# Kernel tuning notes

Hardware: AMD Instinct MI355X
Metric: run time of the kernel (lower is better)

Reference implementation:

```python
import jax, jax.numpy as jnp
import numpy as np


def _dwconv(x, w, pad):
    # depthwise conv, x: [B,C,H,W], w: [C,1,kh,kw]
    return jax.lax.conv_general_dilated(
        x, w, (1, 1), [(pad, pad), (pad, pad)],
        dimension_numbers=('NCHW', 'OIHW', 'NCHW'),
        feature_group_count=x.shape[1])


def _hw_to_wh(x, h, w):
    # rearrange 'b (h w) c -> b (w h) c'
    b, t, c = x.shape
    return x.reshape(b, h, w, c).transpose(0, 2, 1, 3).reshape(b, t, c)


def _wkv(decay, first, k, v):
    # Vision-RWKV WKV: decay/first [C4]; k, v [B, T, C4]
    w_neg = -jnp.exp(decay)  # RUN_CUDA applies w = -exp(w)
    u = first

    def step(carry, kv):
        p, q, o = carry
        kt, vt = kv
        no = jnp.maximum(o, u + kt)
        A = jnp.exp(o - no)
        Bx = jnp.exp(u + kt - no)
        y = (A * p + Bx * vt) / (A * q + Bx)
        no2 = jnp.maximum(o + w_neg, kt)
        A2 = jnp.exp(o + w_neg - no2)
        B2 = jnp.exp(kt - no2)
        return (A2 * p + B2 * vt, A2 * q + B2, no2), y

    Bn, T, C4 = k.shape
    init = (jnp.zeros((Bn, C4), k.dtype), jnp.zeros((Bn, C4), k.dtype),
            jnp.full((Bn, C4), -1e38, k.dtype))
    _, ys = jax.lax.scan(step, init, (jnp.swapaxes(k, 0, 1), jnp.swapaxes(v, 0, 1)))
    return jnp.swapaxes(ys, 0, 1)  # [B, T, C4]


def setup_inputs() -> dict:
    key = jax.random.key(0)
    ks = jax.random.split(key, 16)
    B, H, W, C = 8, 64, 64, 256
    T = H * W
    C4 = 4 * C
    s = 1.0 / np.sqrt(C)
    return {
        'x': jax.random.normal(ks[0], (B, T, C), jnp.float32),
        'alpha': jax.random.normal(ks[1], (4,), jnp.float32) * 0.5,
        'dw1': jax.random.normal(ks[2], (C, 1, 1, 1), jnp.float32) * s,
        'dw3': jax.random.normal(ks[3], (C, 1, 3, 3), jnp.float32) * s,
        'dw5': jax.random.normal(ks[4], (C, 1, 5, 5), jnp.float32) * s,
        'Wk': jax.random.normal(ks[5], (C, C), jnp.float32) * s,
        'Wv': jax.random.normal(ks[6], (C, C), jnp.float32) * s,
        'Wr': jax.random.normal(ks[7], (C, C), jnp.float32) * s,
        'Wf': jax.random.normal(ks[8], (C, C), jnp.float32) * s,
        'bf': jax.random.normal(ks[9], (C,), jnp.float32) * 0.02,
        'Wb': jax.random.normal(ks[10], (C, C), jnp.float32) * s,
        'bb': jax.random.normal(ks[11], (C,), jnp.float32) * 0.02,
        'spatial_decay': jax.random.normal(ks[12], (C4,), jnp.float32),
        'spatial_first': jax.random.normal(ks[13], (C4,), jnp.float32),
        'Wo': jax.random.normal(ks[14], (C, C4), jnp.float32) * (1.0 / np.sqrt(C4)),
        'h': H,
        'w': W,
    }


def reference(x, alpha, dw1, dw3, dw5, Wk, Wv, Wr, Wf, bf, Wb, bb,
              spatial_decay, spatial_first, Wo, h, w):
    B, T, C = x.shape
    # OmniShift (training path): alpha-weighted identity + depthwise 1/3/5 convs
    xi = x.reshape(B, h, w, C).transpose(0, 3, 1, 2)  # [B,C,H,W]
    xsft = (alpha[0] * xi + alpha[1] * _dwconv(xi, dw1, 0)
            + alpha[2] * _dwconv(xi, dw3, 1) + alpha[3] * _dwconv(xi, dw5, 2))
    xf = xsft.transpose(0, 2, 3, 1).reshape(B, T, C)  # [B,T,C]
    k = xf @ Wk.T
    v = xf @ Wv.T
    sr = jax.nn.sigmoid(xf @ Wr.T)
    # 1x1 conv1d over channels == linear with bias
    k1 = k @ Wf.T + bf
    v1 = v @ Wf.T + bf
    k3 = k @ Wb.T + bb
    v3 = v @ Wb.T + bb
    k2 = _hw_to_wh(k1, h, w)
    v2 = _hw_to_wh(v1, h, w)
    k4 = _hw_to_wh(k3, h, w)
    v4 = _hw_to_wh(v3, h, w)
    ks_ = jnp.concatenate([k1, k2, k3, k4], axis=2)  # [B,T,4C]
    vs_ = jnp.concatenate([v1, v2, v3, v4], axis=2)
    srs = jnp.concatenate([sr, sr, sr, sr], axis=2)
    Tf = jnp.asarray(T, x.dtype)
    xs = _wkv(spatial_decay / Tf, spatial_first / Tf, ks_, vs_)
    return (xs * srs) @ Wo.T  # [B,T,C]
```

## Files before the change

### kernel.cpp

```cpp
#include <hip/hip_runtime.h>

typedef __attribute__((ext_vector_type(8))) short bf16x8;
typedef __attribute__((ext_vector_type(4))) float f32x4;
typedef __attribute__((ext_vector_type(4))) unsigned short u16x4;
typedef __attribute__((ext_vector_type(2))) unsigned short u16x2;
typedef __attribute__((ext_vector_type(8))) unsigned short u16x8;

#define GLD16(g, l) __builtin_amdgcn_global_load_lds( \
    (const __attribute__((address_space(1))) void*)(g), \
    (__attribute__((address_space(3))) void*)(l), 16, 0, 0)

__device__ __forceinline__ unsigned short f2bf(float f) {
  unsigned u = __float_as_uint(f);
  unsigned r = u + 0x7FFFu + ((u >> 16) & 1u);
  return (unsigned short)(r >> 16);
}
__device__ __forceinline__ float bf2f(unsigned short h) {
  return __uint_as_float(((unsigned)h) << 16);
}


__global__ void k_weff(const float* __restrict__ alpha,
                       const float* __restrict__ dw1,
                       const float* __restrict__ dw3,
                       const float* __restrict__ dw5,
                       float* __restrict__ weff) {
  int tap = blockIdx.x;
  int c = threadIdx.x;
  int dy = tap / 5, dx = tap % 5;
  float v = alpha[3] * dw5[c * 25 + tap];
  if (dy >= 1 && dy <= 3 && dx >= 1 && dx <= 3)
    v += alpha[2] * dw3[c * 9 + (dy - 1) * 3 + (dx - 1)];
  if (tap == 12) v += alpha[1] * dw1[c] + alpha[0];
  weff[tap * 256 + c] = v;
}

__global__ void k_combine(const float* __restrict__ Wk,
                          const float* __restrict__ Wv,
                          const float* __restrict__ Wr,
                          const float* __restrict__ Wf,
                          const float* __restrict__ Wb,
                          const float* __restrict__ bfv,
                          const float* __restrict__ bbv,
                          short* __restrict__ wcat,
                          float* __restrict__ bias) {
  int mat = blockIdx.x >> 8;
  int i = blockIdx.x & 255;
  int j = threadIdx.x;
  if (mat == 4) {
    wcat[(size_t)(1024 + i) * 256 + j] = (short)f2bf(Wr[i * 256 + j]);
    if (j == 0) bias[1024 + i] = 0.f;
    return;
  }
  const float* Am = (mat & 1) ? Wb : Wf;
  const float* Bm = (mat < 2) ? Wk : Wv;
  const float* arow = Am + i * 256;
  float acc = 0.f;
  for (int m = 0; m < 256; ++m) acc += arow[m] * Bm[m * 256 + j];
  int newrow = ((mat & 1) << 9) + (i << 1) + (mat >> 1);
  wcat[(size_t)newrow * 256 + j] = (short)f2bf(acc);
  if (j == 0) bias[newrow] = (mat & 1) ? bbv[i] : bfv[i];
}

__global__ void k_wo(const float* __restrict__ Wo, short* __restrict__ wob) {
  int i = blockIdx.x * 256 + threadIdx.x;
  wob[i] = (short)f2bf(Wo[i]);
}

__global__ __launch_bounds__(256, 8)
void k_shift(const float* __restrict__ x, const float* __restrict__ weff,
             unsigned short* __restrict__ xf) {
  int c = threadIdx.x;
  int w0 = blockIdx.x * 8;
  int h0 = blockIdx.y * 2;
  int b = blockIdx.z;

  float wg[5][5];
#pragma unroll
  for (int dy = 0; dy < 5; ++dy)
#pragma unroll
    for (int dx = 0; dx < 5; ++dx)
      wg[dy][dx] = weff[(dy * 5 + dx) * 256 + c];

  const float* xb = x + (size_t)b * 4096 * 256 + c;
  int rowoff[6];
  bool rv[6];
#pragma unroll
  for (int r = 0; r < 6; ++r) {
    int y = h0 + r - 2;
    rv[r] = (y >= 0 && y < 64);
    int yc = y < 0 ? 0 : (y > 63 ? 63 : y);
    rowoff[r] = yc * 64 * 256;
  }

  float win[6][8];
#pragma unroll
  for (int j = -2; j <= 1; ++j) {
    int xx = w0 + j;
    int slot = j & 7;
    bool xv = (xx >= 0);
    int xc = xx < 0 ? 0 : xx;
#pragma unroll
    for (int r = 0; r < 6; ++r) {
      float v = xb[rowoff[r] + xc * 256];
      win[r][slot] = (xv && rv[r]) ? v : 0.f;
    }
  }

  unsigned short* xo = xf + ((size_t)b * 4096 + (size_t)h0 * 64) * 256 + c;
#pragma unroll
  for (int ui = 0; ui < 8; ++ui) {
    int w = w0 + ui;
    {
      int xx = w + 2;
      int slot = (ui + 2) & 7;
      bool xv = (xx < 64);
      int xc = xx > 63 ? 63 : xx;
#pragma unroll
      for (int r = 0; r < 6; ++r) {
        float v = xb[rowoff[r] + xc * 256];
        win[r][slot] = (xv && rv[r]) ? v : 0.f;
      }
    }
#pragma unroll
    for (int j = 0; j < 2; ++j) {
      float a0 = 0.f, a1 = 0.f, a2 = 0.f, a3 = 0.f, a4 = 0.f;
#pragma unroll
      for (int dx = 0; dx < 5; ++dx) {
        int slot = (ui - 2 + dx) & 7;
        a0 = fmaf(win[j + 0][slot], wg[0][dx], a0);
        a1 = fmaf(win[j + 1][slot], wg[1][dx], a1);
        a2 = fmaf(win[j + 2][slot], wg[2][dx], a2);
        a3 = fmaf(win[j + 3][slot], wg[3][dx], a3);
        a4 = fmaf(win[j + 4][slot], wg[4][dx], a4);
      }
      xo[((size_t)j * 64 + w) * 256] = f2bf(((a0 + a1) + (a2 + a3)) + a4);
    }
  }
}

template <int EPI, int BM, int BK>
__global__ __launch_bounds__(256, (BK == 128) ? 3 : 4)
void gemm_bt(const short* __restrict__ A, const short* __restrict__ Bm,
             const float* __restrict__ bias,
             void* __restrict__ O0, void* __restrict__ O1,
             int M, int N, int K) {
  constexpr int AE = BM * BK;
  constexpr int MI = BM / 32;
  constexpr int CH = BK / 8;
  constexpr int LA = BM * BK / 2048;
  constexpr int LB = BK / 16;
  constexpr int RW = 132;
  __shared__ __align__(16) short lds[AE + 128 * BK];

  int t = threadIdx.x;
  int lane = t & 63, wv = t >> 6;
  int wr = wv >> 1, wc = wv & 1;
  int m0 = blockIdx.x * BM, n0 = blockIdx.y * 128;
  f32x4 acc[MI][4] = {};

  for (int k0 = 0; k0 < K; k0 += BK) {
#pragma unroll
    for (int i = 0; i < LA; ++i) {
      int cc = t + i * 256;
      int row = cc / CH, kc = cc % CH;
      GLD16(A + (size_t)(m0 + row) * K + k0 + ((kc ^ (row & (CH - 1))) << 3), &lds[cc * 8]);
    }
#pragma unroll
    for (int i = 0; i < LB; ++i) {
      int cc = t + i * 256;
      int row = cc / CH, kc = cc % CH;
      GLD16(Bm + (size_t)(n0 + row) * K + k0 + ((kc ^ (row & (CH - 1))) << 3), &lds[AE + cc * 8]);
    }
    __syncthreads();
#pragma unroll
    for (int kk = 0; kk < BK / 32; ++kk) {
      int ch = kk * 4 + (lane >> 4);
      bf16x8 av[MI], bv[4];
#pragma unroll
      for (int i = 0; i < MI; ++i) {
        int row = wr * (BM / 2) + i * 16 + (lane & 15);
        av[i] = *(const bf16x8*)&lds[row * BK + ((ch ^ (row & (CH - 1))) << 3)];
      }
#pragma unroll
      for (int i = 0; i < 4; ++i) {
        int row = wc * 64 + i * 16 + (lane & 15);
        bv[i] = *(const bf16x8*)&lds[AE + row * BK + ((ch ^ (row & (CH - 1))) << 3)];
      }
#pragma unroll
      for (int mi = 0; mi < MI; ++mi)
#pragma unroll
        for (int ni = 0; ni < 4; ++ni)
          acc[mi][ni] = __builtin_amdgcn_mfma_f32_16x16x32_bf16(av[mi], bv[ni], acc[mi][ni], 0, 0, 0);
    }
    __syncthreads();
  }

  float* fl = (float*)lds;
  float bb[4];
  if (EPI == 0) {
#pragma unroll
    for (int ni = 0; ni < 4; ++ni)
      bb[ni] = bias[n0 + wc * 64 + ni * 16 + (lane & 15)];
  }
  int rrow = t >> 3;
  int colb = (t & 7) * 16;
#pragma unroll
  for (int mi = 0; mi < MI; ++mi) {
    if (mi) __syncthreads();
    {
      int r0 = (lane >> 4) * 4;
#pragma unroll
      for (int ni = 0; ni < 4; ++ni) {
        int colL = wc * 64 + (lane & 15) + ni * 16;
        f32x4 v = acc[mi][ni];
#pragma unroll
        for (int j = 0; j < 4; ++j) {
          float vj = v[j];
          if (EPI == 0) vj += bb[ni];
          fl[(wr * 16 + r0 + j) * RW + colL] = vj;
        }
      }
    }
    __syncthreads();
    float vv[16];
#pragma unroll
    for (int q = 0; q < 4; ++q)
      *(f32x4*)&vv[q * 4] = *(const f32x4*)&fl[rrow * RW + colb + q * 4];
    int grow = m0 + (rrow >> 4) * (BM / 2) + mi * 16 + (rrow & 15);
    if (EPI == 0) {
      u16x8 o0, o1;
      if (n0 < 1024) {
#pragma unroll
        for (int q = 0; q < 8; ++q) { o0[q] = f2bf(vv[q]); o1[q] = f2bf(vv[8 + q]); }
        unsigned short* dst = (unsigned short*)O0 + (size_t)grow * 1024 + n0 + colb;
        *(u16x8*)dst = o0;
        *(u16x8*)(dst + 8) = o1;
      } else {
#pragma unroll
        for (int q = 0; q < 8; ++q) {
          o0[q] = f2bf(1.f / (1.f + __expf(-vv[q])));
          o1[q] = f2bf(1.f / (1.f + __expf(-vv[8 + q])));
        }
        unsigned short* dst = (unsigned short*)O1 + (size_t)grow * 256 + (n0 - 1024) + colb;
        *(u16x8*)dst = o0;
        *(u16x8*)(dst + 8) = o1;
      }
    } else {
      float* dst = (float*)O0 + (size_t)grow * N + n0 + colb;
#pragma unroll
      for (int q = 0; q < 4; ++q) {
        f32x4 ov = {vv[q * 4], vv[q * 4 + 1], vv[q * 4 + 2], vv[q * 4 + 3]};
        *(f32x4*)(dst + q * 4) = ov;
      }
    }
  }
}

__global__ __launch_bounds__(256, 8)
void k_wkv(const unsigned short* __restrict__ kvb, const unsigned short* __restrict__ srb,
           const float* __restrict__ decay, const float* __restrict__ first,
           unsigned short* __restrict__ xssr) {
  const int T = 4096;
  int tid = threadIdx.x;
  int g = tid >> 7;
  int l = tid & 127;
  int c0 = l * 2;
  int tr = blockIdx.y;
  int s = (g << 1) | tr;
  int scol = s * 256;
  int chunk = blockIdx.x;
  int b = blockIdx.z;
  const float invT = 1.0f / 4096.0f;

  float P0 = 0.f, P1 = 0.f, Q0 = 0.f, Q1 = 0.f;
  float D0 = __expf(-__expf(decay[scol + c0] * invT));
  float D1 = __expf(-__expf(decay[scol + c0 + 1] * invT));
  float eu0 = __expf(first[scol + c0] * invT);
  float eu1 = __expf(first[scol + c0 + 1] * invT);

  int t0 = chunk * 32;
  int tstart = t0 >= 16 ? t0 - 16 : 0;
  int tend = t0 + 32;
  const size_t bT = (size_t)b * T;
  const int kvoff = (g << 9) + (c0 << 1);

  auto kvload = [&](int tt) {
    int tok = tr ? (((tt & 63) << 6) | (tt >> 6)) : tt;
    return *(const u16x4*)(kvb + (bT + tok) * 1024 + kvoff);
  };
  auto srload = [&](int tt) {
    return *(const u16x2*)(srb + (bT + tt) * 256 + c0);
  };

  u16x4 kvA = kvload(tstart);
  u16x4 kvB = kvload(tstart + 1);
  u16x2 svA = srload(tstart);
  u16x2 svB = srload(tstart + 1);

  for (int tt = tstart; tt < tend; tt += 2) {
    int tp2 = tt + 2 < tend ? tt + 2 : tend - 1;
    int tp3 = tt + 3 < tend ? tt + 3 : tend - 1;
    u16x4 kvC = kvload(tp2);
    u16x4 kvD = kvload(tp3);
    u16x2 svC = srload(tp2);
    u16x2 svD = srload(tp3);

#pragma unroll
    for (int u = 0; u < 2; ++u) {
      int ti = tt + u;
      u16x4 kv4 = u ? kvB : kvA;
      u16x2 sv = u ? svB : svA;
      float k0 = bf2f(kv4[0]), v0 = bf2f(kv4[1]);
      float k1 = bf2f(kv4[2]), v1 = bf2f(kv4[3]);
      float e0 = __expf(k0), e1 = __expf(k1);
      if (ti >= t0) {
        float t0e = e0 * eu0, t1e = e1 * eu1;
        float y0 = fmaf(t0e, v0, P0) * __builtin_amdgcn_rcpf(Q0 + t0e);
        float y1 = fmaf(t1e, v1, P1) * __builtin_amdgcn_rcpf(Q1 + t1e);
        u16x2 ow;
        ow[0] = f2bf(y0 * bf2f(sv[0]));
        ow[1] = f2bf(y1 * bf2f(sv[1]));
        *(u16x2*)(xssr + (bT + ti) * 1024 + scol + c0) = ow;
      }
      P0 = fmaf(P0, D0, e0 * v0);
      Q0 = fmaf(Q0, D0, e0);
      P1 = fmaf(P1, D1, e1 * v1);
      Q1 = fmaf(Q1, D1, e1);
    }
    kvA = kvC; kvB = kvD;
    svA = svC; svB = svD;
  }
}

extern "C" void kernel_launch(void* const* d_in, const int* in_sizes, int n_in,
                              void* d_out, int out_size, void* d_ws, size_t ws_size,
                              hipStream_t stream) {
  const float* x      = (const float*)d_in[0];
  const float* alpha  = (const float*)d_in[1];
  const float* dw1    = (const float*)d_in[2];
  const float* dw3    = (const float*)d_in[3];
  const float* dw5    = (const float*)d_in[4];
  const float* Wk     = (const float*)d_in[5];
  const float* Wv     = (const float*)d_in[6];
  const float* Wr     = (const float*)d_in[7];
  const float* Wf     = (const float*)d_in[8];
  const float* bfv    = (const float*)d_in[9];
  const float* Wb     = (const float*)d_in[10];
  const float* bbv    = (const float*)d_in[11];
  const float* sdecay = (const float*)d_in[12];
  const float* sfirst = (const float*)d_in[13];
  const float* Wo     = (const float*)d_in[14];
  (void)n_in; (void)out_size; (void)ws_size;

  const int Bn = in_sizes[0] / (4096 * 256);
  const int MT = Bn * 4096;

  char* ws = (char*)d_ws;
  size_t off = 0;
  auto alloc = [&](size_t bytes) {
    void* p = ws + off;
    off += (bytes + 255) & ~(size_t)255;
    return p;
  };
  short* xf            = (short*)alloc((size_t)MT * 256 * 2);
  unsigned short* kv   = (unsigned short*)alloc((size_t)MT * 1024 * 2);
  unsigned short* srb  = (unsigned short*)alloc((size_t)MT * 256 * 2);
  unsigned short* xssr = (unsigned short*)alloc((size_t)MT * 1024 * 2);
  short* wcat          = (short*)alloc((size_t)1280 * 256 * 2);
  float* bias          = (float*)alloc(1280 * 4);
  float* weff          = (float*)alloc(25 * 256 * 4);
  short* wob           = (short*)alloc((size_t)256 * 1024 * 2);

  k_weff<<<25, 256, 0, stream>>>(alpha, dw1, dw3, dw5, weff);
  k_combine<<<1280, 256, 0, stream>>>(Wk, Wv, Wr, Wf, Wb, bfv, bbv, wcat, bias);
  k_wo<<<1024, 256, 0, stream>>>(Wo, wob);
  k_shift<<<dim3(8, 32, Bn), 256, 0, stream>>>(x, weff, (unsigned short*)xf);
  gemm_bt<0, 128, 64><<<dim3(MT / 128, 10), 256, 0, stream>>>(xf, wcat, bias, kv, srb, MT, 1280, 256);
  k_wkv<<<dim3(128, 2, Bn), 256, 0, stream>>>(kv, srb, sdecay, sfirst, xssr);
  gemm_bt<1, 64, 128><<<dim3(MT / 64, 2), 256, 0, stream>>>((const short*)xssr, wob, nullptr, d_out, nullptr, MT, 256, 1024);
}
```

Baseline: 167.3 us.

## Replace LDS-staged GEMM with direct global-to-register MFMA loads and double buffering

Both projection GEMMs stop staging A and B tiles through shared memory with global_load_lds and barriers. Each wave now loads its MFMA fragments straight from global memory into registers, using a two-stage register double buffer that overlaps the next k-slice's loads with the current MFMAs. Shared memory is kept only for the epilogue transpose. The output GEMM also changes its tile from 64 to 128 rows, which halves its block count. The risk is that operands no longer shared across waves are fetched redundantly from global/L2, with less coalesced 16-byte accesses and higher register pressure.

```diff
diff --git a/kernel.cpp b/kernel.cpp
--- a/kernel.cpp
+++ b/kernel.cpp
@@ -5,10 +5,6 @@
 typedef __attribute__((ext_vector_type(4))) unsigned short u16x4;
 typedef __attribute__((ext_vector_type(2))) unsigned short u16x2;
 typedef __attribute__((ext_vector_type(8))) unsigned short u16x8;
-
-#define GLD16(g, l) __builtin_amdgcn_global_load_lds( \
-    (const __attribute__((address_space(1))) void*)(g), \
-    (__attribute__((address_space(3))) void*)(l), 16, 0, 0)
 
 __device__ __forceinline__ unsigned short f2bf(float f) {
   unsigned u = __float_as_uint(f);
@@ -139,64 +135,55 @@
   }
 }
 
-template <int EPI, int BM, int BK>
-__global__ __launch_bounds__(256, (BK == 128) ? 3 : 4)
-void gemm_bt(const short* __restrict__ A, const short* __restrict__ Bm,
-             const float* __restrict__ bias,
-             void* __restrict__ O0, void* __restrict__ O1,
-             int M, int N, int K) {
-  constexpr int AE = BM * BK;
-  constexpr int MI = BM / 32;
-  constexpr int CH = BK / 8;
-  constexpr int LA = BM * BK / 2048;
-  constexpr int LB = BK / 16;
+template <int EPI, int KDIM>
+__global__ __launch_bounds__(256, 3)
+void gemm_direct(const short* __restrict__ A, const short* __restrict__ Bm,
+                 const float* __restrict__ bias,
+                 void* __restrict__ O0, void* __restrict__ O1, int N) {
+  constexpr int K = KDIM;
+  constexpr int NK = K / 32;
   constexpr int RW = 132;
-  __shared__ __align__(16) short lds[AE + 128 * BK];
+  __shared__ __align__(16) float fl[32 * RW];
 
   int t = threadIdx.x;
   int lane = t & 63, wv = t >> 6;
   int wr = wv >> 1, wc = wv & 1;
-  int m0 = blockIdx.x * BM, n0 = blockIdx.y * 128;
-  f32x4 acc[MI][4] = {};
-
-  for (int k0 = 0; k0 < K; k0 += BK) {
-#pragma unroll
-    for (int i = 0; i < LA; ++i) {
-      int cc = t + i * 256;
-      int row = cc / CH, kc = cc % CH;
-      GLD16(A + (size_t)(m0 + row) * K + k0 + ((kc ^ (row & (CH - 1))) << 3), &lds[cc * 8]);
-    }
-#pragma unroll
-    for (int i = 0; i < LB; ++i) {
-      int cc = t + i * 256;
-      int row = cc / CH, kc = cc % CH;
-      GLD16(Bm + (size_t)(n0 + row) * K + k0 + ((kc ^ (row & (CH - 1))) << 3), &lds[AE + cc * 8]);
-    }
-    __syncthreads();
-#pragma unroll
-    for (int kk = 0; kk < BK / 32; ++kk) {
-      int ch = kk * 4 + (lane >> 4);
-      bf16x8 av[MI], bv[4];
-#pragma unroll
-      for (int i = 0; i < MI; ++i) {
-        int row = wr * (BM / 2) + i * 16 + (lane & 15);
-        av[i] = *(const bf16x8*)&lds[row * BK + ((ch ^ (row & (CH - 1))) << 3)];
-      }
-#pragma unroll
-      for (int i = 0; i < 4; ++i) {
-        int row = wc * 64 + i * 16 + (lane & 15);
-        bv[i] = *(const bf16x8*)&lds[AE + row * BK + ((ch ^ (row & (CH - 1))) << 3)];
-      }
-#pragma unroll
-      for (int mi = 0; mi < MI; ++mi)
-#pragma unroll
-        for (int ni = 0; ni < 4; ++ni)
-          acc[mi][ni] = __builtin_amdgcn_mfma_f32_16x16x32_bf16(av[mi], bv[ni], acc[mi][ni], 0, 0, 0);
-    }
-    __syncthreads();
-  }
-
-  float* fl = (float*)lds;
+  int m0 = blockIdx.x * 128, n0 = blockIdx.y * 128;
+  f32x4 acc[4][4] = {};
+
+  const short* Ap = A + (size_t)(m0 + wr * 64 + (lane & 15)) * K + (lane >> 4) * 8;
+  const short* Bp = Bm + (size_t)(n0 + wc * 64 + (lane & 15)) * K + (lane >> 4) * 8;
+
+  bf16x8 aA[4], bA[4], aB[4], bB[4];
+
+#define LOADF(av, bv, kk)                                              \
+  _Pragma("unroll")                                                    \
+  for (int i = 0; i < 4; ++i) {                                        \
+    av[i] = *(const bf16x8*)(Ap + (size_t)i * 16 * K + (kk) * 32);     \
+    bv[i] = *(const bf16x8*)(Bp + (size_t)i * 16 * K + (kk) * 32);     \
+  }
+#define MM(av, bv)                                                     \
+  _Pragma("unroll")                                                    \
+  for (int mi = 0; mi < 4; ++mi) {                                     \
+    _Pragma("unroll")                                                  \
+    for (int ni = 0; ni < 4; ++ni)                                     \
+      acc[mi][ni] = __builtin_amdgcn_mfma_f32_16x16x32_bf16(           \
+          av[mi], bv[ni], acc[mi][ni], 0, 0, 0);                       \
+  }
+
+  LOADF(aA, bA, 0);
+  for (int kk = 0; kk < NK - 2; kk += 2) {
+    LOADF(aB, bB, kk + 1);
+    MM(aA, bA);
+    LOADF(aA, bA, kk + 2);
+    MM(aB, bB);
+  }
+  LOADF(aB, bB, NK - 1);
+  MM(aA, bA);
+  MM(aB, bB);
+#undef LOADF
+#undef MM
+
   float bb[4];
   if (EPI == 0) {
 #pragma unroll
@@ -206,7 +193,7 @@
   int rrow = t >> 3;
   int colb = (t & 7) * 16;
 #pragma unroll
-  for (int mi = 0; mi < MI; ++mi) {
+  for (int mi = 0; mi < 4; ++mi) {
     if (mi) __syncthreads();
     {
       int r0 = (lane >> 4) * 4;
@@ -227,7 +214,7 @@
 #pragma unroll
     for (int q = 0; q < 4; ++q)
       *(f32x4*)&vv[q * 4] = *(const f32x4*)&fl[rrow * RW + colb + q * 4];
-    int grow = m0 + (rrow >> 4) * (BM / 2) + mi * 16 + (rrow & 15);
+    int grow = m0 + (rrow >> 4) * 64 + mi * 16 + (rrow & 15);
     if (EPI == 0) {
       u16x8 o0, o1;
       if (n0 < 1024) {
@@ -376,7 +363,9 @@
   k_combine<<<1280, 256, 0, stream>>>(Wk, Wv, Wr, Wf, Wb, bfv, bbv, wcat, bias);
   k_wo<<<1024, 256, 0, stream>>>(Wo, wob);
   k_shift<<<dim3(8, 32, Bn), 256, 0, stream>>>(x, weff, (unsigned short*)xf);
-  gemm_bt<0, 128, 64><<<dim3(MT / 128, 10), 256, 0, stream>>>(xf, wcat, bias, kv, srb, MT, 1280, 256);
+  gemm_direct<0, 256><<<dim3(MT / 128, 10), 256, 0, stream>>>(
+      xf, wcat, bias, kv, srb, 1280);
   k_wkv<<<dim3(128, 2, Bn), 256, 0, stream>>>(kv, srb, sdecay, sfirst, xssr);
-  gemm_bt<1, 64, 128><<<dim3(MT / 64, 2), 256, 0, stream>>>((const short*)xssr, wob, nullptr, d_out, nullptr, MT, 256, 1024);
-}
+  gemm_direct<1, 1024><<<dim3(MT / 128, 2), 256, 0, stream>>>(
+      (const short*)xssr, wob, nullptr, d_out, nullptr, 256);
+}
```

Result: slower. 254.3 us (+52.0%).

## Keep full-K A tile resident in LDS and sweep all N tiles per block

Applied to the files above, without the earlier changes.

Replaces the first projection GEMM with a dedicated kernel. Each block loads its 128-row A tile (full K=256) into LDS once, then loops over the ten 128-column B tiles, prefetching the next B tile while the current epilogue runs. The epilogue goes through an LDS staging buffer so bias add, bf16 conversion and sigmoid are written as coalesced 16-byte stores. This removes the tenfold re-read of A across column blocks, at the cost of about 145KB of LDS per block, which allows only one 4-wave block per CU and gives little latency hiding during the MFMA phase.

```diff
diff --git a/kernel.cpp b/kernel.cpp
--- a/kernel.cpp
+++ b/kernel.cpp
@@ -135,6 +135,117 @@
         a4 = fmaf(win[j + 4][slot], wg[4][dx], a4);
       }
       xo[((size_t)j * 64 + w) * 256] = f2bf(((a0 + a1) + (a2 + a3)) + a4);
+    }
+  }
+}
+
+__global__ __launch_bounds__(256, 1)
+void k_gemm1(const short* __restrict__ A, const short* __restrict__ Bm,
+             const float* __restrict__ bias,
+             unsigned short* __restrict__ kv, unsigned short* __restrict__ srb) {
+  __shared__ __align__(16) short AB[65536];
+  __shared__ __align__(16) float flb[4][16 * 66];
+
+  int t = threadIdx.x;
+  int lane = t & 63, wv = t >> 6;
+  int wr = wv >> 1, wc = wv & 1;
+  int m0 = blockIdx.x * 128;
+
+#pragma unroll
+  for (int i = 0; i < 16; ++i) {
+    int cc = t + i * 256;
+    int row = cc >> 5, kc = cc & 31;
+    GLD16(A + (size_t)(m0 + row) * 256 + ((kc ^ (row & 31)) << 3), &AB[cc * 8]);
+  }
+#pragma unroll
+  for (int i = 0; i < 16; ++i) {
+    int cc = t + i * 256;
+    int row = cc >> 5, kc = cc & 31;
+    GLD16(Bm + (size_t)row * 256 + ((kc ^ (row & 31)) << 3), &AB[32768 + cc * 8]);
+  }
+  asm volatile("s_waitcnt vmcnt(0)" ::: "memory");
+  __builtin_amdgcn_s_barrier();
+
+  float* flw = flb[wv];
+
+#pragma unroll 1
+  for (int nt = 0; nt < 10; ++nt) {
+    int n0 = nt * 128;
+    if (nt) {
+      asm volatile("s_waitcnt vmcnt(8)" ::: "memory");
+      __builtin_amdgcn_s_barrier();
+    }
+    float bb[4];
+#pragma unroll
+    for (int ni = 0; ni < 4; ++ni)
+      bb[ni] = bias[n0 + wc * 64 + ni * 16 + (lane & 15)];
+
+    f32x4 acc[4][4] = {};
+#pragma unroll
+    for (int kk = 0; kk < 8; ++kk) {
+      int ch = kk * 4 + (lane >> 4);
+      bf16x8 av[4], bv[4];
+#pragma unroll
+      for (int i = 0; i < 4; ++i) {
+        int row = wr * 64 + i * 16 + (lane & 15);
+        av[i] = *(const bf16x8*)&AB[row * 256 + ((ch ^ (row & 31)) << 3)];
+      }
+#pragma unroll
+      for (int i = 0; i < 4; ++i) {
+        int row = wc * 64 + i * 16 + (lane & 15);
+        bv[i] = *(const bf16x8*)&AB[32768 + row * 256 + ((ch ^ (row & 31)) << 3)];
+      }
+#pragma unroll
+      for (int mi = 0; mi < 4; ++mi)
+#pragma unroll
+        for (int ni = 0; ni < 4; ++ni)
+          acc[mi][ni] = __builtin_amdgcn_mfma_f32_16x16x32_bf16(av[mi], bv[ni], acc[mi][ni], 0, 0, 0);
+    }
+    asm volatile("s_waitcnt lgkmcnt(0)" ::: "memory");
+    __builtin_amdgcn_s_barrier();
+
+    if (nt < 9) {
+      int n1 = n0 + 128;
+#pragma unroll
+      for (int i = 0; i < 16; ++i) {
+        int cc = t + i * 256;
+        int row = cc >> 5, kc = cc & 31;
+        GLD16(Bm + (size_t)(n1 + row) * 256 + ((kc ^ (row & 31)) << 3),
+              &AB[32768 + cc * 8]);
+      }
+    }
+
+#pragma unroll
+    for (int mi = 0; mi < 4; ++mi) {
+      int g = lane >> 4;
+#pragma unroll
+      for (int ni = 0; ni < 4; ++ni) {
+        f32x4 v = acc[mi][ni];
+#pragma unroll
+        for (int j = 0; j < 4; ++j)
+          flw[(g * 4 + j) * 66 + ni * 16 + (lane & 15)] = v[j] + bb[ni];
+      }
+      asm volatile("s_waitcnt lgkmcnt(0)" ::: "memory");
+#pragma unroll
+      for (int rp = 0; rp < 2; ++rp) {
+        int r = (lane >> 3) + rp * 8;
+        int c0 = (lane & 7) * 8;
+        float vv[8];
+#pragma unroll
+        for (int q = 0; q < 4; ++q)
+          *(float2*)&vv[q * 2] = *(const float2*)&flw[r * 66 + c0 + q * 2];
+        int grow = m0 + wr * 64 + mi * 16 + r;
+        u16x8 o;
+        if (n0 < 1024) {
+#pragma unroll
+          for (int q = 0; q < 8; ++q) o[q] = f2bf(vv[q]);
+          *(u16x8*)(kv + (size_t)grow * 1024 + n0 + wc * 64 + c0) = o;
+        } else {
+#pragma unroll
+          for (int q = 0; q < 8; ++q) o[q] = f2bf(1.f / (1.f + __expf(-vv[q])));
+          *(u16x8*)(srb + (size_t)grow * 256 + (n0 - 1024) + wc * 64 + c0) = o;
+        }
+      }
     }
   }
 }
@@ -376,7 +487,7 @@
   k_combine<<<1280, 256, 0, stream>>>(Wk, Wv, Wr, Wf, Wb, bfv, bbv, wcat, bias);
   k_wo<<<1024, 256, 0, stream>>>(Wo, wob);
   k_shift<<<dim3(8, 32, Bn), 256, 0, stream>>>(x, weff, (unsigned short*)xf);
-  gemm_bt<0, 128, 64><<<dim3(MT / 128, 10), 256, 0, stream>>>(xf, wcat, bias, kv, srb, MT, 1280, 256);
+  k_gemm1<<<MT / 128, 256, 0, stream>>>(xf, wcat, bias, kv, srb);
   k_wkv<<<dim3(128, 2, Bn), 256, 0, stream>>>(kv, srb, sdecay, sfirst, xssr);
   gemm_bt<1, 64, 128><<<dim3(MT / 64, 2), 256, 0, stream>>>((const short*)xssr, wob, nullptr, d_out, nullptr, MT, 256, 1024);
 }
```

New measurement: 172.8 us. +3.3%, slower.
